# Kernel optimization log

Measured on AMD Instinct MI355X. Metric: run time of the kernel, lower is better.

## Reference

```python
import jax, jax.numpy as jnp
import numpy as np

MAX_SEQLEN = 2048  # static max sequence length (flash varlen APIs take this as a host arg)


def setup_inputs() -> dict:
    key = jax.random.key(0)
    k1, k2, k3 = jax.random.split(key, 3)
    T, H, D = 8192, 8, 128
    B = 4
    q = jax.random.normal(k1, (T, H, D), dtype=jnp.float32)
    k = jax.random.normal(k2, (T, H, D), dtype=jnp.float32)
    v = jax.random.normal(k3, (T, H, D), dtype=jnp.float32)
    cu = (jnp.arange(B + 1, dtype=jnp.int32) * (T // B))  # [0,2048,4096,6144,8192]
    return {"q": q, "k": k, "v": v, "cu_seqlens_q": cu, "cu_seqlens_k": cu}


def reference(q, k, v, cu_seqlens_q, cu_seqlens_k):
    """Varlen (ragged) multi-head attention, non-causal (flash_attn varlen default).

    q,k,v: [T, H, D] packed over sequences; cu_seqlens: [B+1] boundaries.
    Gathers each sequence into a padded [B, S, H, D] layout, computes
    per-sequence softmax(q k^T / sqrt(D)) v with padding masked, then
    scatters back to packed [T, H, D].
    """
    T, H, D = q.shape
    B = cu_seqlens_q.shape[0] - 1
    S = MAX_SEQLEN
    scale = 1.0 / jnp.sqrt(jnp.asarray(D, q.dtype))

    pos = jnp.arange(S)
    q_start = cu_seqlens_q[:-1]
    k_start = cu_seqlens_k[:-1]
    q_len = jnp.diff(cu_seqlens_q)  # [B]
    k_len = jnp.diff(cu_seqlens_k)

    q_idx = jnp.clip(q_start[:, None] + pos[None, :], 0, T - 1)  # [B, S]
    k_idx = jnp.clip(k_start[:, None] + pos[None, :], 0, T - 1)
    q_valid = pos[None, :] < q_len[:, None]  # [B, S]
    k_valid = pos[None, :] < k_len[:, None]

    qb = q[q_idx]  # [B, S, H, D]
    kb = k[k_idx]
    vb = v[k_idx]

    scores = jnp.einsum('bqhd,bkhd->bhqk', qb, kb) * scale  # [B, H, S, S]
    neg = jnp.asarray(-1e30, scores.dtype)
    scores = jnp.where(k_valid[:, None, None, :], scores, neg)
    attn = jax.nn.softmax(scores, axis=-1)
    ob = jnp.einsum('bhqk,bkhd->bqhd', attn, vb)  # [B, S, H, D]

    # zero padded query rows, then scatter-add back to packed layout
    ob = jnp.where(q_valid[:, :, None, None], ob, 0.0)
    out = jnp.zeros_like(q).at[q_idx.reshape(-1)].add(ob.reshape(B * S, H, D))
    return out
```

## Files before the change

### kernel.cpp

```cpp
#include <hip/hip_runtime.h>
#include <hip/hip_bf16.h>
#include <stdint.h>

#define HH 8
#define DD 128
#define MAXSEQ 2048
#define QBLK 128

typedef float f32x16 __attribute__((ext_vector_type(16)));
typedef short s16x8 __attribute__((ext_vector_type(8)));

__device__ __forceinline__ unsigned short f2bf(float x) {
  union { float f; uint32_t u; } v; v.f = x;
  uint32_t u = v.u;
  return (unsigned short)((u + 0x7FFFu + ((u >> 16) & 1u)) >> 16);
}

__global__ void zero_rows(const int* __restrict__ cuq, float* __restrict__ out, int T, int B) {
  const int t = blockIdx.x * blockDim.x + threadIdx.x;
  if (t >= T) return;
  bool covered = false;
  for (int b = 0; b < B; ++b) {
    const int s = cuq[b];
    const int len = min(cuq[b + 1] - s, MAXSEQ);
    if (t >= s && t < s + len) covered = true;
  }
  if (!covered) {
    float4* p = (float4*)(out + (size_t)t * HH * DD);
#pragma unroll 4
    for (int i = 0; i < HH * DD / 4; ++i) p[i] = float4{0.f, 0.f, 0.f, 0.f};
  }
}

__global__ void kconv2(const float* __restrict__ k, unsigned short* __restrict__ kb2, int T) {
  const int TBc = T >> 5;
  const int total = TBc * HH * 512;
  const int u = blockIdx.x * blockDim.x + threadIdx.x;
  if (u >= total) return;
  const int lp = u & 63;
  const int key = lp & 31, hi = lp >> 5;
  int r = u >> 6;
  const int s = r & 7; r >>= 3;
  const int tb = r % TBc;
  const int h = r / TBc;
  const int t = tb * 32 + key;
  const int d = s * 16 + hi * 8;
  const float* src = k + ((size_t)t * HH + h) * DD + d;
  float4 a = *(const float4*)src;
  float4 c = *(const float4*)(src + 4);
  union { unsigned short us[8]; uint4 q; } w;
  w.us[0] = f2bf(a.x); w.us[1] = f2bf(a.y); w.us[2] = f2bf(a.z); w.us[3] = f2bf(a.w);
  w.us[4] = f2bf(c.x); w.us[5] = f2bf(c.y); w.us[6] = f2bf(c.z); w.us[7] = f2bf(c.w);
  *(uint4*)(kb2 + (size_t)u * 8) = w.q;
}

__global__ void vconv(const float* __restrict__ v, unsigned short* __restrict__ vb2, int T) {
  const int TBc = T >> 5;
  const int total = TBc * HH * 512;
  const int u = blockIdx.x * blockDim.x + threadIdx.x;
  if (u >= total) return;
  const int lo = u & 31;
  const int hi = (u >> 5) & 1;
  const int i = (u >> 6) & 7;
  const int dt = i & 3, ks2 = i >> 2;
  int r = u >> 9;
  const int tb = r % TBc;
  const int h = r / TBc;
  const int t0 = tb * 32 + ks2 * 16 + hi * 8;
  const int d = dt * 32 + lo;
  union { unsigned short us[8]; uint4 q; } w;
#pragma unroll
  for (int j = 0; j < 8; ++j)
    w.us[j] = f2bf(v[((size_t)(t0 + j) * HH + h) * DD + d]);
  *(uint4*)(vb2 + (size_t)u * 8) = w.q;
}

__global__ __launch_bounds__(256, 2)
void attn_main(const float* __restrict__ q,
               const unsigned short* __restrict__ kb2,
               const unsigned short* __restrict__ vb2,
               const int* __restrict__ cuq,
               const int* __restrict__ cuk,
               float* __restrict__ out,
               int T, int BH) {
  const int TBc = T >> 5;
  const int bid = blockIdx.x;
  const int bh = bid % BH;
  const int qt = bid / BH;
  const int b = bh / HH, h = bh % HH;
  const int qs = cuq[b], qe = cuq[b + 1];
  const int ks = cuk[b], ke = cuk[b + 1];
  const int nq = min(qe - qs, MAXSEQ);
  const int nk = min(ke - ks, MAXSEQ);
  if (qt * QBLK >= nq || nk <= 0) return;

  const int tid = threadIdx.x;
  const int wave = tid >> 6;
  const int lane = tid & 63;
  const int lo = lane & 31;
  const int hi = lane >> 5;

  const int kb32 = ks >> 5;
  const unsigned short* kb2h = kb2 + (size_t)h * TBc * 4096;
  const unsigned short* vb2h = vb2 + (size_t)h * TBc * 4096;

  const float SC = (1.0f / 11.313708498984761f) * 1.4426950408889634f;
  const int qrow = qt * QBLK + wave * 32 + lo;
  const int qg = qs + min(qrow, nq - 1);
  const float* qp = q + ((size_t)qg * HH + h) * DD;
  s16x8 qf[8];
#pragma unroll
  for (int s = 0; s < 8; ++s) {
    const float* p0 = qp + s * 16 + hi * 8;
    float4 a = *(const float4*)(p0);
    float4 c = *(const float4*)(p0 + 4);
    union { unsigned short us[8]; s16x8 v; } u;
    u.us[0] = f2bf(a.x * SC); u.us[1] = f2bf(a.y * SC);
    u.us[2] = f2bf(a.z * SC); u.us[3] = f2bf(a.w * SC);
    u.us[4] = f2bf(c.x * SC); u.us[5] = f2bf(c.y * SC);
    u.us[6] = f2bf(c.z * SC); u.us[7] = f2bf(c.w * SC);
    qf[s] = u.v;
  }

  f32x16 Oa[4];
#pragma unroll
  for (int i = 0; i < 4; ++i)
#pragma unroll
    for (int r = 0; r < 16; ++r) Oa[i][r] = 0.0f;

  float l_run = 0.0f;
  const float SHIFT = 8.0f;

  const int nkt = (nk + 31) / 32;

  auto loadK = [&](s16x8(&kf)[8], int stile) {
    const size_t base = (size_t)min(stile, TBc - 1) * 4096;
#pragma unroll
    for (int s = 0; s < 8; ++s)
      kf[s] = *(const s16x8*)(kb2h + base + s * 512 + lane * 8);
  };
  auto loadV = [&](s16x8(&vf)[8], int stile) {
    const size_t base = (size_t)min(stile, TBc - 1) * 4096;
#pragma unroll
    for (int i = 0; i < 8; ++i)
      vf[i] = *(const s16x8*)(vb2h + base + i * 512 + lane * 8);
  };

  s16x8 kf[8], vf[8];
  loadK(kf, kb32);
  loadV(vf, kb32);

  for (int kt = 0; kt < nkt; ++kt) {
    f32x16 st;
#pragma unroll
    for (int r = 0; r < 16; ++r) st[r] = 0.0f;
    __builtin_amdgcn_s_setprio(1);
#pragma unroll
    for (int s = 0; s < 8; ++s)
      st = __builtin_amdgcn_mfma_f32_32x32x16_bf16(kf[s], qf[s], st, 0, 0, 0);
    __builtin_amdgcn_s_setprio(0);

    if (kt + 1 < nkt) loadK(kf, kb32 + kt + 1);

    const int lim = nk - kt * 32;
    if (lim < 32) {
#pragma unroll
      for (int r = 0; r < 16; ++r) {
        const int base = (r & 3) + 8 * (r >> 2) + 4 * hi;
        if (base >= lim) st[r] = -__builtin_inff();
      }
    }

    float p[16];
    float psum = 0.0f;
#pragma unroll
    for (int r = 0; r < 16; ++r) {
      p[r] = __builtin_amdgcn_exp2f(st[r] - SHIFT);
      psum += p[r];
    }
    l_run += psum;

    uint32_t ownu[8];
#pragma unroll
    for (int c = 0; c < 4; ++c) {
      uint32_t w0, w1;
      asm("v_cvt_pk_bf16_f32 %0, %1, %2" : "=v"(w0) : "v"(p[4 * c + 0]), "v"(p[4 * c + 1]));
      asm("v_cvt_pk_bf16_f32 %0, %1, %2" : "=v"(w1) : "v"(p[4 * c + 2]), "v"(p[4 * c + 3]));
      ownu[c * 2 + 0] = w0;
      ownu[c * 2 + 1] = w1;
    }

    __builtin_amdgcn_s_setprio(1);
#pragma unroll
    for (int ks2 = 0; ks2 < 2; ++ks2) {
      uint32_t a0 = ownu[4 * ks2 + 0], b0 = ownu[4 * ks2 + 2];
      uint32_t a1 = ownu[4 * ks2 + 1], b1 = ownu[4 * ks2 + 3];
      asm("v_permlane32_swap_b32 %0, %1" : "+v"(a0), "+v"(b0));
      asm("v_permlane32_swap_b32 %0, %1" : "+v"(a1), "+v"(b1));
      union { uint32_t u[4]; s16x8 v; } pu;
      pu.u[0] = a0; pu.u[1] = a1; pu.u[2] = b0; pu.u[3] = b1;
#pragma unroll
      for (int dt = 0; dt < 4; ++dt)
        Oa[dt] = __builtin_amdgcn_mfma_f32_32x32x16_bf16(pu.v, vf[ks2 * 4 + dt], Oa[dt], 0, 0, 0);
    }
    __builtin_amdgcn_s_setprio(0);

    if (kt + 1 < nkt) loadV(vf, kb32 + kt + 1);
  }

  l_run += __shfl_xor(l_run, 32);
  const float linv = 1.0f / l_run;
#pragma unroll
  for (int r = 0; r < 16; ++r) {
    const int src = (r & 3) + 8 * (r >> 2) + 4 * hi;
    const float li = __shfl(linv, src);
    const int qirow = qt * QBLK + wave * 32 + src;
    if (qirow < nq) {
      float* op = out + ((size_t)(qs + qirow) * HH + h) * DD;
      op[0 * 32 + lo] = Oa[0][r] * li;
      op[1 * 32 + lo] = Oa[1][r] * li;
      op[2 * 32 + lo] = Oa[2][r] * li;
      op[3 * 32 + lo] = Oa[3][r] * li;
    }
  }
}

extern "C" void kernel_launch(void* const* d_in, const int* in_sizes, int n_in,
                              void* d_out, int out_size, void* d_ws, size_t ws_size,
                              hipStream_t stream) {
  const float* q = (const float*)d_in[0];
  const float* k = (const float*)d_in[1];
  const float* v = (const float*)d_in[2];
  const int* cuq = (const int*)d_in[3];
  const int* cuk = (const int*)d_in[4];
  float* out = (float*)d_out;
  const int T = in_sizes[0] / (HH * DD);
  const int B = in_sizes[3] - 1;

  unsigned short* kb2 = (unsigned short*)d_ws;
  unsigned short* vb2 = kb2 + (size_t)T * HH * DD;
  const size_t need = (size_t)T * HH * DD * 2 * 2;
  if (ws_size < need) return;

  {
    zero_rows<<<(T + 255) / 256, 256, 0, stream>>>(cuq, out, T, B);
  }
  {
    const int total = (T >> 5) * HH * 512;
    kconv2<<<(total + 255) / 256, 256, 0, stream>>>(k, kb2, T);
    vconv<<<(total + 255) / 256, 256, 0, stream>>>(v, vb2, T);
  }
  {
    const int BH = B * HH;
    const int scap = MAXSEQ < T ? MAXSEQ : T;
    const int qtiles = (scap + QBLK - 1) / QBLK;
    attn_main<<<BH * qtiles, 256, 0, stream>>>(q, kb2, vb2, cuq, cuk, out, T, BH);
  }
}
```

Before: 121.2 us.

## Software-pipeline QK and PV across key tiles and fuse K/V conversion kernels

Restructures the attention loop so the QK^T MFMA for the next key tile is issued alongside softmax and PV of the previous tile, using two alternating score accumulators. Masking is moved to only the final tile, and the fixed exponent shift is removed. K and V bf16 conversion kernels are merged into one launch to cut launch overhead. Dropping the shift raises the risk of exp overflow for large scores, and the extra score buffer adds register pressure.

```diff
diff --git a/kernel.cpp b/kernel.cpp
--- a/kernel.cpp
+++ b/kernel.cpp
@@ -32,47 +32,43 @@
   }
 }
 
-__global__ void kconv2(const float* __restrict__ k, unsigned short* __restrict__ kb2, int T) {
+__global__ void kvconv(const float* __restrict__ k, const float* __restrict__ v,
+                       unsigned short* __restrict__ kb2, unsigned short* __restrict__ vb2, int T) {
   const int TBc = T >> 5;
   const int total = TBc * HH * 512;
-  const int u = blockIdx.x * blockDim.x + threadIdx.x;
-  if (u >= total) return;
-  const int lp = u & 63;
-  const int key = lp & 31, hi = lp >> 5;
-  int r = u >> 6;
-  const int s = r & 7; r >>= 3;
-  const int tb = r % TBc;
-  const int h = r / TBc;
-  const int t = tb * 32 + key;
-  const int d = s * 16 + hi * 8;
-  const float* src = k + ((size_t)t * HH + h) * DD + d;
-  float4 a = *(const float4*)src;
-  float4 c = *(const float4*)(src + 4);
-  union { unsigned short us[8]; uint4 q; } w;
-  w.us[0] = f2bf(a.x); w.us[1] = f2bf(a.y); w.us[2] = f2bf(a.z); w.us[3] = f2bf(a.w);
-  w.us[4] = f2bf(c.x); w.us[5] = f2bf(c.y); w.us[6] = f2bf(c.z); w.us[7] = f2bf(c.w);
-  *(uint4*)(kb2 + (size_t)u * 8) = w.q;
-}
-
-__global__ void vconv(const float* __restrict__ v, unsigned short* __restrict__ vb2, int T) {
-  const int TBc = T >> 5;
-  const int total = TBc * HH * 512;
-  const int u = blockIdx.x * blockDim.x + threadIdx.x;
-  if (u >= total) return;
-  const int lo = u & 31;
-  const int hi = (u >> 5) & 1;
-  const int i = (u >> 6) & 7;
-  const int dt = i & 3, ks2 = i >> 2;
-  int r = u >> 9;
-  const int tb = r % TBc;
-  const int h = r / TBc;
-  const int t0 = tb * 32 + ks2 * 16 + hi * 8;
-  const int d = dt * 32 + lo;
-  union { unsigned short us[8]; uint4 q; } w;
-#pragma unroll
-  for (int j = 0; j < 8; ++j)
-    w.us[j] = f2bf(v[((size_t)(t0 + j) * HH + h) * DD + d]);
-  *(uint4*)(vb2 + (size_t)u * 8) = w.q;
+  int u = blockIdx.x * blockDim.x + threadIdx.x;
+  if (u < total) {
+    const int lp = u & 63;
+    const int key = lp & 31, hi = lp >> 5;
+    int r = u >> 6;
+    const int s = r & 7; r >>= 3;
+    const int tb = r % TBc;
+    const int h = r / TBc;
+    const int t = tb * 32 + key;
+    const int d = s * 16 + hi * 8;
+    const float* src = k + ((size_t)t * HH + h) * DD + d;
+    float4 a = *(const float4*)src;
+    float4 c = *(const float4*)(src + 4);
+    union { unsigned short us[8]; uint4 q; } w;
+    w.us[0] = f2bf(a.x); w.us[1] = f2bf(a.y); w.us[2] = f2bf(a.z); w.us[3] = f2bf(a.w);
+    w.us[4] = f2bf(c.x); w.us[5] = f2bf(c.y); w.us[6] = f2bf(c.z); w.us[7] = f2bf(c.w);
+    *(uint4*)(kb2 + (size_t)u * 8) = w.q;
+  } else if ((u -= total) < total) {
+    const int lo = u & 31;
+    const int hi = (u >> 5) & 1;
+    const int i = (u >> 6) & 7;
+    const int dt = i & 3, ks2 = i >> 2;
+    int r = u >> 9;
+    const int tb = r % TBc;
+    const int h = r / TBc;
+    const int t0 = tb * 32 + ks2 * 16 + hi * 8;
+    const int d = dt * 32 + lo;
+    union { unsigned short us[8]; uint4 q; } w;
+#pragma unroll
+    for (int j = 0; j < 8; ++j)
+      w.us[j] = f2bf(v[((size_t)(t0 + j) * HH + h) * DD + d]);
+    *(uint4*)(vb2 + (size_t)u * 8) = w.q;
+  }
 }
 
 __global__ __launch_bounds__(256, 2)
@@ -129,29 +125,26 @@
     for (int r = 0; r < 16; ++r) Oa[i][r] = 0.0f;
 
   float l_run = 0.0f;
-  const float SHIFT = 8.0f;
-
   const int nkt = (nk + 31) / 32;
 
-  auto loadK = [&](s16x8(&kf)[8], int stile) {
-    const size_t base = (size_t)min(stile, TBc - 1) * 4096;
+  s16x8 kf[8], vf[8];
+  f32x16 stA, stB;
+  uint32_t pu[8];
+
+  auto loadK = [&](int stile) {
+    const unsigned short* base = kb2h + (size_t)stile * 4096 + lane * 8;
 #pragma unroll
     for (int s = 0; s < 8; ++s)
-      kf[s] = *(const s16x8*)(kb2h + base + s * 512 + lane * 8);
-  };
-  auto loadV = [&](s16x8(&vf)[8], int stile) {
-    const size_t base = (size_t)min(stile, TBc - 1) * 4096;
+      kf[s] = *(const s16x8*)(base + s * 512);
+  };
+  auto loadV = [&](int stile) {
+    const unsigned short* base = vb2h + (size_t)stile * 4096 + lane * 8;
 #pragma unroll
     for (int i = 0; i < 8; ++i)
-      vf[i] = *(const s16x8*)(vb2h + base + i * 512 + lane * 8);
-  };
-
-  s16x8 kf[8], vf[8];
-  loadK(kf, kb32);
-  loadV(vf, kb32);
-
-  for (int kt = 0; kt < nkt; ++kt) {
-    f32x16 st;
+      vf[i] = *(const s16x8*)(base + i * 512);
+  };
+
+  auto QK = [&](f32x16& st) {
 #pragma unroll
     for (int r = 0; r < 16; ++r) st[r] = 0.0f;
     __builtin_amdgcn_s_setprio(1);
@@ -159,27 +152,17 @@
     for (int s = 0; s < 8; ++s)
       st = __builtin_amdgcn_mfma_f32_32x32x16_bf16(kf[s], qf[s], st, 0, 0, 0);
     __builtin_amdgcn_s_setprio(0);
-
-    if (kt + 1 < nkt) loadK(kf, kb32 + kt + 1);
-
-    const int lim = nk - kt * 32;
-    if (lim < 32) {
-#pragma unroll
-      for (int r = 0; r < 16; ++r) {
-        const int base = (r & 3) + 8 * (r >> 2) + 4 * hi;
-        if (base >= lim) st[r] = -__builtin_inff();
-      }
-    }
-
+  };
+
+  auto SMPACK = [&](f32x16& st) {
     float p[16];
-    float psum = 0.0f;
-#pragma unroll
-    for (int r = 0; r < 16; ++r) {
-      p[r] = __builtin_amdgcn_exp2f(st[r] - SHIFT);
-      psum += p[r];
-    }
-    l_run += psum;
-
+#pragma unroll
+    for (int r = 0; r < 16; ++r) p[r] = __builtin_amdgcn_exp2f(st[r]);
+    float s01 = (p[0] + p[1]) + (p[2] + p[3]);
+    float s23 = (p[4] + p[5]) + (p[6] + p[7]);
+    float s45 = (p[8] + p[9]) + (p[10] + p[11]);
+    float s67 = (p[12] + p[13]) + (p[14] + p[15]);
+    l_run += (s01 + s23) + (s45 + s67);
     uint32_t ownu[8];
 #pragma unroll
     for (int c = 0; c < 4; ++c) {
@@ -189,24 +172,68 @@
       ownu[c * 2 + 0] = w0;
       ownu[c * 2 + 1] = w1;
     }
-
-    __builtin_amdgcn_s_setprio(1);
 #pragma unroll
     for (int ks2 = 0; ks2 < 2; ++ks2) {
       uint32_t a0 = ownu[4 * ks2 + 0], b0 = ownu[4 * ks2 + 2];
       uint32_t a1 = ownu[4 * ks2 + 1], b1 = ownu[4 * ks2 + 3];
       asm("v_permlane32_swap_b32 %0, %1" : "+v"(a0), "+v"(b0));
       asm("v_permlane32_swap_b32 %0, %1" : "+v"(a1), "+v"(b1));
-      union { uint32_t u[4]; s16x8 v; } pu;
-      pu.u[0] = a0; pu.u[1] = a1; pu.u[2] = b0; pu.u[3] = b1;
+      pu[4 * ks2 + 0] = a0; pu[4 * ks2 + 1] = a1;
+      pu[4 * ks2 + 2] = b0; pu[4 * ks2 + 3] = b1;
+    }
+  };
+
+  auto PV = [&]() {
+    __builtin_amdgcn_s_setprio(1);
+#pragma unroll
+    for (int ks2 = 0; ks2 < 2; ++ks2) {
+      union { uint32_t u[4]; s16x8 v; } pv_;
+      pv_.u[0] = pu[4 * ks2 + 0]; pv_.u[1] = pu[4 * ks2 + 1];
+      pv_.u[2] = pu[4 * ks2 + 2]; pv_.u[3] = pu[4 * ks2 + 3];
 #pragma unroll
       for (int dt = 0; dt < 4; ++dt)
-        Oa[dt] = __builtin_amdgcn_mfma_f32_32x32x16_bf16(pu.v, vf[ks2 * 4 + dt], Oa[dt], 0, 0, 0);
+        Oa[dt] = __builtin_amdgcn_mfma_f32_32x32x16_bf16(pv_.v, vf[ks2 * 4 + dt], Oa[dt], 0, 0, 0);
     }
     __builtin_amdgcn_s_setprio(0);
-
-    if (kt + 1 < nkt) loadV(vf, kb32 + kt + 1);
-  }
+  };
+
+  auto MASK = [&](f32x16& st) {
+    const int lim = nk - (nkt - 1) * 32;
+    if (lim < 32) {
+#pragma unroll
+      for (int r = 0; r < 16; ++r) {
+        const int base = (r & 3) + 8 * (r >> 2) + 4 * hi;
+        if (base >= lim) st[r] = -__builtin_inff();
+      }
+    }
+  };
+
+  auto ITER = [&](int t, f32x16& stPrev, f32x16& stCur) {
+    loadV(kb32 + t - 1);
+    SMPACK(stPrev);
+    QK(stCur);
+    if (t + 1 < nkt) loadK(kb32 + t + 1);
+    PV();
+  };
+
+  auto EPI = [&](f32x16& stLast) {
+    loadV(kb32 + nkt - 1);
+    MASK(stLast);
+    SMPACK(stLast);
+    PV();
+  };
+
+  loadK(kb32);
+  QK(stA);
+  if (nkt > 1) loadK(kb32 + 1);
+
+  int t = 1;
+  for (; t + 1 < nkt; t += 2) {
+    ITER(t, stA, stB);
+    ITER(t + 1, stB, stA);
+  }
+  if (t < nkt) { ITER(t, stA, stB); EPI(stB); }
+  else EPI(stA);
 
   l_run += __shfl_xor(l_run, 32);
   const float linv = 1.0f / l_run;
@@ -247,8 +274,7 @@
   }
   {
     const int total = (T >> 5) * HH * 512;
-    kconv2<<<(total + 255) / 256, 256, 0, stream>>>(k, kb2, T);
-    vconv<<<(total + 255) / 256, 256, 0, stream>>>(v, vb2, T);
+    kvconv<<<(2 * total + 255) / 256, 256, 0, stream>>>(k, v, kb2, vb2, T);
   }
   {
     const int BH = B * HH;
```

New measurement: 115.0 us. -5.1%, faster.

## Stage K/V tiles in LDS via async global-to-LDS double buffering

Applied to the files above, without the earlier changes.

The attention kernel now copies 64-key K and V tiles into shared memory with global_load_lds double buffering, so all four waves in a block share one copy instead of each loading K/V into registers. Each iteration processes two 32-key subtiles, and V is stored in a permuted layout so the permlane32 swap is no longer needed. The two conversion kernels are merged into one launch, and the fixed exp shift of 8 is removed. In exchange it uses 64KB of LDS per block and a __syncthreads per tile, which may cut occupancy. Dropping the shift also changes numerics: with no running max, exp2 of large scores could overflow.

```diff
diff --git a/kernel.cpp b/kernel.cpp
--- a/kernel.cpp
+++ b/kernel.cpp
@@ -14,6 +14,11 @@
   union { float f; uint32_t u; } v; v.f = x;
   uint32_t u = v.u;
   return (unsigned short)((u + 0x7FFFu + ((u >> 16) & 1u)) >> 16);
+}
+
+__device__ __forceinline__ void gload_lds16(const unsigned short* g, unsigned short* l) {
+  __builtin_amdgcn_global_load_lds((const __attribute__((address_space(1))) void*)g,
+                                   (__attribute__((address_space(3))) void*)l, 16, 0, 0);
 }
 
 __global__ void zero_rows(const int* __restrict__ cuq, float* __restrict__ out, int T, int B) {
@@ -32,47 +37,45 @@
   }
 }
 
-__global__ void kconv2(const float* __restrict__ k, unsigned short* __restrict__ kb2, int T) {
+__global__ void kvconv(const float* __restrict__ k, const float* __restrict__ v,
+                       unsigned short* __restrict__ kb2, unsigned short* __restrict__ vb2, int T) {
   const int TBc = T >> 5;
   const int total = TBc * HH * 512;
-  const int u = blockIdx.x * blockDim.x + threadIdx.x;
-  if (u >= total) return;
-  const int lp = u & 63;
-  const int key = lp & 31, hi = lp >> 5;
-  int r = u >> 6;
-  const int s = r & 7; r >>= 3;
-  const int tb = r % TBc;
-  const int h = r / TBc;
-  const int t = tb * 32 + key;
-  const int d = s * 16 + hi * 8;
-  const float* src = k + ((size_t)t * HH + h) * DD + d;
-  float4 a = *(const float4*)src;
-  float4 c = *(const float4*)(src + 4);
-  union { unsigned short us[8]; uint4 q; } w;
-  w.us[0] = f2bf(a.x); w.us[1] = f2bf(a.y); w.us[2] = f2bf(a.z); w.us[3] = f2bf(a.w);
-  w.us[4] = f2bf(c.x); w.us[5] = f2bf(c.y); w.us[6] = f2bf(c.z); w.us[7] = f2bf(c.w);
-  *(uint4*)(kb2 + (size_t)u * 8) = w.q;
-}
-
-__global__ void vconv(const float* __restrict__ v, unsigned short* __restrict__ vb2, int T) {
-  const int TBc = T >> 5;
-  const int total = TBc * HH * 512;
-  const int u = blockIdx.x * blockDim.x + threadIdx.x;
-  if (u >= total) return;
-  const int lo = u & 31;
-  const int hi = (u >> 5) & 1;
-  const int i = (u >> 6) & 7;
-  const int dt = i & 3, ks2 = i >> 2;
-  int r = u >> 9;
-  const int tb = r % TBc;
-  const int h = r / TBc;
-  const int t0 = tb * 32 + ks2 * 16 + hi * 8;
-  const int d = dt * 32 + lo;
-  union { unsigned short us[8]; uint4 q; } w;
-#pragma unroll
-  for (int j = 0; j < 8; ++j)
-    w.us[j] = f2bf(v[((size_t)(t0 + j) * HH + h) * DD + d]);
-  *(uint4*)(vb2 + (size_t)u * 8) = w.q;
+  int u = blockIdx.x * blockDim.x + threadIdx.x;
+  if (u < total) {
+    const int lp = u & 63;
+    const int key = lp & 31, hi = lp >> 5;
+    int r = u >> 6;
+    const int c = r & 7; r >>= 3;
+    const int tb = r % TBc;
+    const int h = r / TBc;
+    const int t = tb * 32 + key;
+    const int d = c * 16 + hi * 8;
+    const float* src = k + ((size_t)t * HH + h) * DD + d;
+    float4 a = *(const float4*)src;
+    float4 cc = *(const float4*)(src + 4);
+    union { unsigned short us[8]; uint4 q; } w;
+    w.us[0] = f2bf(a.x); w.us[1] = f2bf(a.y); w.us[2] = f2bf(a.z); w.us[3] = f2bf(a.w);
+    w.us[4] = f2bf(cc.x); w.us[5] = f2bf(cc.y); w.us[6] = f2bf(cc.z); w.us[7] = f2bf(cc.w);
+    *(uint4*)(kb2 + (size_t)u * 8) = w.q;
+  } else if ((u -= total) < total) {
+    const int lo = u & 31;
+    const int hi = (u >> 5) & 1;
+    const int i = (u >> 6) & 7;
+    const int dt = i & 3, ks2 = i >> 2;
+    int r = u >> 9;
+    const int tb = r % TBc;
+    const int h = r / TBc;
+    const int d = dt * 32 + lo;
+    union { unsigned short us[8]; uint4 q; } w;
+#pragma unroll
+    for (int j = 0; j < 8; ++j) {
+      const int phys = 16 * ks2 + ((j < 4) ? (4 * hi + j) : (8 + 4 * hi + (j - 4)));
+      const int t = tb * 32 + phys;
+      w.us[j] = f2bf(v[((size_t)t * HH + h) * DD + d]);
+    }
+    *(uint4*)(vb2 + (size_t)u * 8) = w.q;
+  }
 }
 
 __global__ __launch_bounds__(256, 2)
@@ -83,6 +86,8 @@
                const int* __restrict__ cuk,
                float* __restrict__ out,
                int T, int BH) {
+  extern __shared__ __align__(16) unsigned short smem[];
+
   const int TBc = T >> 5;
   const int bid = blockIdx.x;
   const int bh = bid % BH;
@@ -99,6 +104,7 @@
   const int lane = tid & 63;
   const int lo = lane & 31;
   const int hi = lane >> 5;
+  const int wub = (tid & ~63) * 8;
 
   const int kb32 = ks >> 5;
   const unsigned short* kb2h = kb2 + (size_t)h * TBc * 4096;
@@ -110,16 +116,16 @@
   const float* qp = q + ((size_t)qg * HH + h) * DD;
   s16x8 qf[8];
 #pragma unroll
-  for (int s = 0; s < 8; ++s) {
-    const float* p0 = qp + s * 16 + hi * 8;
+  for (int c = 0; c < 8; ++c) {
+    const float* p0 = qp + c * 16 + hi * 8;
     float4 a = *(const float4*)(p0);
-    float4 c = *(const float4*)(p0 + 4);
+    float4 cc = *(const float4*)(p0 + 4);
     union { unsigned short us[8]; s16x8 v; } u;
     u.us[0] = f2bf(a.x * SC); u.us[1] = f2bf(a.y * SC);
     u.us[2] = f2bf(a.z * SC); u.us[3] = f2bf(a.w * SC);
-    u.us[4] = f2bf(c.x * SC); u.us[5] = f2bf(c.y * SC);
-    u.us[6] = f2bf(c.z * SC); u.us[7] = f2bf(c.w * SC);
-    qf[s] = u.v;
+    u.us[4] = f2bf(cc.x * SC); u.us[5] = f2bf(cc.y * SC);
+    u.us[6] = f2bf(cc.z * SC); u.us[7] = f2bf(cc.w * SC);
+    qf[c] = u.v;
   }
 
   f32x16 Oa[4];
@@ -129,83 +135,108 @@
     for (int r = 0; r < 16; ++r) Oa[i][r] = 0.0f;
 
   float l_run = 0.0f;
-  const float SHIFT = 8.0f;
-
-  const int nkt = (nk + 31) / 32;
-
-  auto loadK = [&](s16x8(&kf)[8], int stile) {
-    const size_t base = (size_t)min(stile, TBc - 1) * 4096;
-#pragma unroll
-    for (int s = 0; s < 8; ++s)
-      kf[s] = *(const s16x8*)(kb2h + base + s * 512 + lane * 8);
+  const int nkt = (nk + 63) / 64;
+
+  auto stage = [&](int buf, int kt) {
+    unsigned short* Kd = smem + buf * 8192;
+    unsigned short* Vd = smem + 16384 + buf * 8192;
+#pragma unroll
+    for (int r = 0; r < 4; ++r) {
+      const int u = r * 256 + tid;
+      const int tb = min(kb32 + 2 * kt + (u >> 9), TBc - 1);
+      gload_lds16(kb2h + (size_t)tb * 4096 + (size_t)(u & 511) * 8, Kd + (size_t)(r * 256) * 8 + wub);
+    }
+#pragma unroll
+    for (int r = 0; r < 4; ++r) {
+      const int u = r * 256 + tid;
+      const int tb = min(kb32 + 2 * kt + (u >> 9), TBc - 1);
+      gload_lds16(vb2h + (size_t)tb * 4096 + (size_t)(u & 511) * 8, Vd + (size_t)(r * 256) * 8 + wub);
+    }
   };
-  auto loadV = [&](s16x8(&vf)[8], int stile) {
-    const size_t base = (size_t)min(stile, TBc - 1) * 4096;
-#pragma unroll
-    for (int i = 0; i < 8; ++i)
-      vf[i] = *(const s16x8*)(vb2h + base + i * 512 + lane * 8);
-  };
-
-  s16x8 kf[8], vf[8];
-  loadK(kf, kb32);
-  loadV(vf, kb32);
-
+
+  stage(0, 0);
+  __syncthreads();
+
+  int buf = 0;
   for (int kt = 0; kt < nkt; ++kt) {
-    f32x16 st;
-#pragma unroll
-    for (int r = 0; r < 16; ++r) st[r] = 0.0f;
-    __builtin_amdgcn_s_setprio(1);
-#pragma unroll
-    for (int s = 0; s < 8; ++s)
-      st = __builtin_amdgcn_mfma_f32_32x32x16_bf16(kf[s], qf[s], st, 0, 0, 0);
-    __builtin_amdgcn_s_setprio(0);
-
-    if (kt + 1 < nkt) loadK(kf, kb32 + kt + 1);
-
-    const int lim = nk - kt * 32;
-    if (lim < 32) {
+    if (kt + 1 < nkt) stage(buf ^ 1, kt + 1);
+
+    const unsigned short* Kb = smem + buf * 8192;
+    const unsigned short* Vb = smem + 16384 + buf * 8192;
+
+    f32x16 st0, st1;
+#pragma unroll
+    for (int r = 0; r < 16; ++r) { st0[r] = 0.0f; st1[r] = 0.0f; }
+    {
+      s16x8 kfA[8], kfB[8];
+#pragma unroll
+      for (int c = 0; c < 8; ++c) kfA[c] = *(const s16x8*)(Kb + c * 512 + lane * 8);
+#pragma unroll
+      for (int c = 0; c < 8; ++c) kfB[c] = *(const s16x8*)(Kb + 4096 + c * 512 + lane * 8);
+      __builtin_amdgcn_s_setprio(1);
+#pragma unroll
+      for (int c = 0; c < 8; ++c) {
+        st0 = __builtin_amdgcn_mfma_f32_32x32x16_bf16(kfA[c], qf[c], st0, 0, 0, 0);
+        st1 = __builtin_amdgcn_mfma_f32_32x32x16_bf16(kfB[c], qf[c], st1, 0, 0, 0);
+      }
+      __builtin_amdgcn_s_setprio(0);
+    }
+
+    const int lim = nk - kt * 64;
+    if (lim < 64) {
 #pragma unroll
       for (int r = 0; r < 16; ++r) {
-        const int base = (r & 3) + 8 * (r >> 2) + 4 * hi;
-        if (base >= lim) st[r] = -__builtin_inff();
+        const int a = (r & 3) + 8 * (r >> 2) + 4 * hi;
+        if (a >= lim) st0[r] = -__builtin_inff();
+        if (a + 32 >= lim) st1[r] = -__builtin_inff();
       }
     }
 
-    float p[16];
-    float psum = 0.0f;
+    float p[32];
 #pragma unroll
     for (int r = 0; r < 16; ++r) {
-      p[r] = __builtin_amdgcn_exp2f(st[r] - SHIFT);
-      psum += p[r];
-    }
-    l_run += psum;
-
-    uint32_t ownu[8];
-#pragma unroll
-    for (int c = 0; c < 4; ++c) {
+      p[r] = __builtin_amdgcn_exp2f(st0[r]);
+      p[16 + r] = __builtin_amdgcn_exp2f(st1[r]);
+    }
+    float ps = 0.f;
+#pragma unroll
+    for (int r = 0; r < 32; r += 4) ps += (p[r] + p[r + 1]) + (p[r + 2] + p[r + 3]);
+    l_run += ps;
+
+    uint32_t pw[16];
+#pragma unroll
+    for (int g = 0; g < 8; ++g) {
       uint32_t w0, w1;
-      asm("v_cvt_pk_bf16_f32 %0, %1, %2" : "=v"(w0) : "v"(p[4 * c + 0]), "v"(p[4 * c + 1]));
-      asm("v_cvt_pk_bf16_f32 %0, %1, %2" : "=v"(w1) : "v"(p[4 * c + 2]), "v"(p[4 * c + 3]));
-      ownu[c * 2 + 0] = w0;
-      ownu[c * 2 + 1] = w1;
-    }
-
-    __builtin_amdgcn_s_setprio(1);
-#pragma unroll
-    for (int ks2 = 0; ks2 < 2; ++ks2) {
-      uint32_t a0 = ownu[4 * ks2 + 0], b0 = ownu[4 * ks2 + 2];
-      uint32_t a1 = ownu[4 * ks2 + 1], b1 = ownu[4 * ks2 + 3];
-      asm("v_permlane32_swap_b32 %0, %1" : "+v"(a0), "+v"(b0));
-      asm("v_permlane32_swap_b32 %0, %1" : "+v"(a1), "+v"(b1));
-      union { uint32_t u[4]; s16x8 v; } pu;
-      pu.u[0] = a0; pu.u[1] = a1; pu.u[2] = b0; pu.u[3] = b1;
-#pragma unroll
-      for (int dt = 0; dt < 4; ++dt)
-        Oa[dt] = __builtin_amdgcn_mfma_f32_32x32x16_bf16(pu.v, vf[ks2 * 4 + dt], Oa[dt], 0, 0, 0);
-    }
-    __builtin_amdgcn_s_setprio(0);
-
-    if (kt + 1 < nkt) loadV(vf, kb32 + kt + 1);
+      asm("v_cvt_pk_bf16_f32 %0, %1, %2" : "=v"(w0) : "v"(p[4 * g + 0]), "v"(p[4 * g + 1]));
+      asm("v_cvt_pk_bf16_f32 %0, %1, %2" : "=v"(w1) : "v"(p[4 * g + 2]), "v"(p[4 * g + 3]));
+      pw[2 * g] = w0;
+      pw[2 * g + 1] = w1;
+    }
+
+    {
+      s16x8 vf[16];
+#pragma unroll
+      for (int i = 0; i < 8; ++i) vf[i] = *(const s16x8*)(Vb + i * 512 + lane * 8);
+#pragma unroll
+      for (int i = 0; i < 8; ++i) vf[8 + i] = *(const s16x8*)(Vb + 4096 + i * 512 + lane * 8);
+      __builtin_amdgcn_s_setprio(1);
+#pragma unroll
+      for (int Hk = 0; Hk < 4; ++Hk) {
+        union { uint32_t u[4]; s16x8 v; } pa;
+        pa.u[0] = pw[4 * Hk + 0]; pa.u[1] = pw[4 * Hk + 1];
+        pa.u[2] = pw[4 * Hk + 2]; pa.u[3] = pw[4 * Hk + 3];
+        const int H = Hk >> 1, ks2 = Hk & 1;
+#pragma unroll
+        for (int dt = 0; dt < 4; ++dt)
+          Oa[dt] = __builtin_amdgcn_mfma_f32_32x32x16_bf16(pa.v, vf[H * 8 + ks2 * 4 + dt], Oa[dt], 0, 0, 0);
+      }
+      __builtin_amdgcn_s_setprio(0);
+    }
+
+    if (kt + 1 < nkt) {
+      __syncthreads();
+      buf ^= 1;
+    }
   }
 
   l_run += __shfl_xor(l_run, 32);
@@ -247,13 +278,12 @@
   }
   {
     const int total = (T >> 5) * HH * 512;
-    kconv2<<<(total + 255) / 256, 256, 0, stream>>>(k, kb2, T);
-    vconv<<<(total + 255) / 256, 256, 0, stream>>>(v, vb2, T);
+    kvconv<<<(2 * total + 255) / 256, 256, 0, stream>>>(k, v, kb2, vb2, T);
   }
   {
     const int BH = B * HH;
     const int scap = MAXSEQ < T ? MAXSEQ : T;
     const int qtiles = (scap + QBLK - 1) / QBLK;
-    attn_main<<<BH * qtiles, 256, 0, stream>>>(q, kb2, vb2, cuq, cuk, out, T, BH);
-  }
-}
+    attn_main<<<BH * qtiles, 256, 65536, stream>>>(q, kb2, vb2, cuq, cuk, out, T, BH);
+  }
+}
```

After: 104.1 us. -14.1%, faster.
